# Optimization experiments

Measured on AMD Instinct MI355X. Metric: run time of the kernel, lower is better.

Reference implementation:

```python
import jax, jax.numpy as jnp
import numpy as np

B, T, N, F = 16, 12, 1000, 64
K_CHEB, OUT = 3, 64


def setup_inputs() -> dict:
    key = jax.random.key(0)
    k1, k2, k3, k4 = jax.random.split(key, 4)
    x = jax.random.normal(k1, (B, T, N, F), dtype=jnp.float32)
    SAtt = jax.random.uniform(k2, (B, N, N), dtype=jnp.float32)
    cheb = jax.random.normal(k3, (K_CHEB, N, N), dtype=jnp.float32) * 0.05
    Theta = jax.random.normal(k4, (K_CHEB, F, OUT), dtype=jnp.float32) * 0.05
    return {"x": x, "SAtt": SAtt, "cheb": cheb, "Theta": Theta}


def reference(x, SAtt, cheb, Theta):
    # Attention-masked Chebyshev polynomials: A[b,k,i,j] = cheb[k,i,j] * SAtt[b,i,j]
    A = cheb[None, :, :, :] * SAtt[:, None, :, :]          # (B,K,N,N)
    # rhs[b,t,k,i,f] = sum_j A[b,k,j,i] * x[b,t,j,f]  (transpose of A in original code)
    rhs = jnp.einsum('bkji,btjf->btkif', A, x)             # (B,T,K,N,F)
    # accumulate over k with per-k feature transform Theta[k]
    out = jnp.einsum('btkif,kfo->btio', rhs, Theta)        # (B,T,N,OUT)
    return jax.nn.relu(out)
```

## Files before the change

kernel.cpp:

```cpp
#include <hip/hip_runtime.h>

#define B_  16
#define T_  12
#define N_  1000
#define F_  64
#define KC  3
#define O_  64
#define NP  1024
#define KP  (KC * NP)
#define CC  (T_ * O_)

typedef __bf16 bf16x8 __attribute__((ext_vector_type(8)));
typedef float  f32x4  __attribute__((ext_vector_type(4)));

__device__ __forceinline__ unsigned short f2bf(float f) {
  __bf16 h = (__bf16)f;
  return __builtin_bit_cast(unsigned short, h);
}

__device__ __forceinline__ void gl_lds16(const void* g, void* l) {
  __builtin_amdgcn_global_load_lds(
      (const __attribute__((address_space(1))) unsigned int*)g,
      (__attribute__((address_space(3))) unsigned int*)l,
      16, 0, 0);
}

__global__ __launch_bounds__(256) void k_build_as(
    const float* __restrict__ SAtt, const float* __restrict__ cheb,
    unsigned short* __restrict__ ASt) {
  __shared__ unsigned short prod[KC][64][66];
  const int tid = threadIdx.x;
  const int b = blockIdx.z, ib = blockIdx.x * 64, jb = blockIdx.y * 64;

  const int ii4 = (tid & 15) * 4, jr = tid >> 4;
#pragma unroll
  for (int p = 0; p < 4; ++p) {
    const int jj = p * 16 + jr;
    const int gj = jb + jj;
    const int gjc = gj < N_ ? gj : N_ - 1;
    const int gi = ib + ii4;
    const bool iok = gi < N_;
    const bool ok = iok && (gj < N_);
    float4 s4 = make_float4(0.f, 0.f, 0.f, 0.f);
    if (iok) s4 = *(const float4*)&SAtt[((size_t)b * N_ + gjc) * N_ + gi];
#pragma unroll
    for (int k = 0; k < KC; ++k) {
      float4 c4 = make_float4(0.f, 0.f, 0.f, 0.f);
      if (iok) c4 = *(const float4*)&cheb[((size_t)k * N_ + gjc) * N_ + gi];
      ushort2 lo, hi;
      lo.x = ok ? f2bf(c4.x * s4.x) : (unsigned short)0;
      lo.y = ok ? f2bf(c4.y * s4.y) : (unsigned short)0;
      hi.x = ok ? f2bf(c4.z * s4.z) : (unsigned short)0;
      hi.y = ok ? f2bf(c4.w * s4.w) : (unsigned short)0;
      *(ushort2*)&prod[k][jj][ii4]     = lo;
      *(ushort2*)&prod[k][jj][ii4 + 2] = hi;
    }
  }
  __syncthreads();

  const int j8 = (tid & 7) * 8, i0 = tid >> 3;
#pragma unroll
  for (int p = 0; p < 2; ++p) {
    const int iw = p * 32 + i0;
#pragma unroll
    for (int k = 0; k < KC; ++k) {
      unsigned short v[8];
#pragma unroll
      for (int m = 0; m < 8; ++m) v[m] = prod[k][j8 + m][iw];
      *(uint4*)&ASt[((size_t)(b * NP + ib + iw) * KC + k) * NP + jb + j8] =
          *(uint4*)v;
    }
  }
}

__global__ __launch_bounds__(256) void k_build_y(
    const float* __restrict__ x, const float* __restrict__ Theta,
    unsigned short* __restrict__ Yt) {
  __shared__ unsigned short thl[KC][64][72];
  __shared__ unsigned short xl[128][72];
  __shared__ unsigned short ot[64][136];
  const int tid = threadIdx.x;
  const int bt = blockIdx.y;
  const int jb = blockIdx.x * 128;

#pragma unroll
  for (int it = 0; it < 12; ++it) {
    const int e = (tid + it * 256) * 4;
    const int k = e >> 12, f = (e >> 6) & 63, o0 = e & 63;
    const float4 v = *(const float4*)&Theta[e];
    thl[k][o0 + 0][f] = f2bf(v.x);
    thl[k][o0 + 1][f] = f2bf(v.y);
    thl[k][o0 + 2][f] = f2bf(v.z);
    thl[k][o0 + 3][f] = f2bf(v.w);
  }
  const float* xrow = x + ((size_t)bt * N_ + jb) * F_;
#pragma unroll
  for (int p = 0; p < 8; ++p) {
    const int i4 = tid + p * 256;
    const int fl = i4 * 4, j = fl >> 6, f = fl & 63;
    float4 v;
    if (jb + j < N_) v = ((const float4*)xrow)[i4];
    else             v = make_float4(0.f, 0.f, 0.f, 0.f);
    ushort4 u;
    u.x = f2bf(v.x); u.y = f2bf(v.y); u.z = f2bf(v.z); u.w = f2bf(v.w);
    *(ushort4*)&xl[j][f] = u;
  }
  __syncthreads();

  const int w = tid >> 6, l = tid & 63, quad = l >> 4, lr = l & 15;
  const int o16 = tid >> 4, j8v = (tid & 15) * 8;
#pragma unroll
  for (int k = 0; k < KC; ++k) {
    f32x4 acc[4][2];
#pragma unroll
    for (int mi = 0; mi < 4; ++mi)
#pragma unroll
      for (int ni = 0; ni < 2; ++ni)
        acc[mi][ni] = (f32x4){0.f, 0.f, 0.f, 0.f};
#pragma unroll
    for (int ks = 0; ks < 2; ++ks) {
      const int fo = ks * 32 + quad * 8;
      bf16x8 a[4], bb[2];
#pragma unroll
      for (int mi = 0; mi < 4; ++mi)
        a[mi] = *(const bf16x8*)&thl[k][mi * 16 + lr][fo];
#pragma unroll
      for (int ni = 0; ni < 2; ++ni)
        bb[ni] = *(const bf16x8*)&xl[w * 32 + ni * 16 + lr][fo];
#pragma unroll
      for (int mi = 0; mi < 4; ++mi)
#pragma unroll
        for (int ni = 0; ni < 2; ++ni)
          acc[mi][ni] = __builtin_amdgcn_mfma_f32_16x16x32_bf16(
              a[mi], bb[ni], acc[mi][ni], 0, 0, 0);
    }
    __syncthreads();
#pragma unroll
    for (int mi = 0; mi < 4; ++mi)
#pragma unroll
      for (int ni = 0; ni < 2; ++ni)
#pragma unroll
        for (int r = 0; r < 4; ++r)
          ot[mi * 16 + quad * 4 + r][w * 32 + ni * 16 + lr] =
              f2bf(acc[mi][ni][r]);
    __syncthreads();
#pragma unroll
    for (int oo = 0; oo < 4; ++oo) {
      const int o = oo * 16 + o16;
      const uint4 v = *(const uint4*)&ot[o][j8v];
      *(uint4*)&Yt[((size_t)(bt * O_ + o) * KC + k) * NP + jb + j8v] = v;
    }
  }
}

__global__ __launch_bounds__(256, 2) void k_gemm(
    const unsigned short* __restrict__ ASt, const unsigned short* __restrict__ Yt,
    float* __restrict__ out) {
  __shared__ unsigned short Al[128 * 64];
  __shared__ unsigned short Bl[128 * 64];
  const int tid = threadIdx.x;
  const int bid = blockIdx.x;
  const int xcd = bid & 7, s = bid >> 3;
  const int b = xcd * 2 + (s / 48);
  const int r48 = s % 48;
  const int ib = (r48 / 6) * 128, cb = (r48 % 6) * 128;

  const unsigned short* Abase = ASt + ((size_t)b * NP + ib) * KP;
  const unsigned short* Bbase = Yt + ((size_t)b * CC + cb) * KP;
  const int w = tid >> 6, l = tid & 63, quad = l >> 4, lr = l & 15;
  const int wr = w & 1, wc = w >> 1;
  const int lrow = l >> 3, lchunk = l & 7;
  const int src_chunk = lchunk ^ lrow;
  const int p0 = quad ^ (lr & 7);

  f32x4 acc[4][4];
#pragma unroll
  for (int mi = 0; mi < 4; ++mi)
#pragma unroll
    for (int ci = 0; ci < 4; ++ci)
      acc[mi][ci] = (f32x4){0.f, 0.f, 0.f, 0.f};

  for (int kt = 0; kt < KP / 64; ++kt) {
    __syncthreads();
    const int k0 = kt * 64;
#pragma unroll
    for (int s4 = 0; s4 < 4; ++s4) {
      const int row = w * 32 + s4 * 8;
      gl_lds16(Abase + (size_t)(row + lrow) * KP + k0 + src_chunk * 8,
               &Al[row * 64]);
      gl_lds16(Bbase + (size_t)(row + lrow) * KP + k0 + src_chunk * 8,
               &Bl[row * 64]);
    }
    __syncthreads();
#pragma unroll
    for (int ks = 0; ks < 2; ++ks) {
      const int pc = (p0 ^ (ks * 4)) * 8;
      bf16x8 a[4], bb[4];
#pragma unroll
      for (int mi = 0; mi < 4; ++mi)
        a[mi] = *(const bf16x8*)&Al[(wr * 64 + mi * 16 + lr) * 64 + pc];
#pragma unroll
      for (int ci = 0; ci < 4; ++ci)
        bb[ci] = *(const bf16x8*)&Bl[(wc * 64 + ci * 16 + lr) * 64 + pc];
#pragma unroll
      for (int mi = 0; mi < 4; ++mi)
#pragma unroll
        for (int ci = 0; ci < 4; ++ci)
          acc[mi][ci] = __builtin_amdgcn_mfma_f32_16x16x32_bf16(
              a[mi], bb[ci], acc[mi][ci], 0, 0, 0);
    }
  }

#pragma unroll
  for (int mi = 0; mi < 4; ++mi) {
    const int i = ib + wr * 64 + mi * 16 + quad * 4;
#pragma unroll
    for (int ci = 0; ci < 4; ++ci) {
      const int c = cb + wc * 64 + ci * 16 + lr;
      const int t = c >> 6, o = c & 63;
#pragma unroll
      for (int r = 0; r < 4; ++r) {
        if (i + r < N_) {
          const float v = acc[mi][ci][r];
          out[((size_t)(b * T_ + t) * N_ + (i + r)) * O_ + o] = v > 0.f ? v : 0.f;
        }
      }
    }
  }
}

extern "C" void kernel_launch(void* const* d_in, const int* in_sizes, int n_in,
                              void* d_out, int out_size, void* d_ws, size_t ws_size,
                              hipStream_t stream) {
  const float* x     = (const float*)d_in[0];
  const float* SAtt  = (const float*)d_in[1];
  const float* cheb  = (const float*)d_in[2];
  const float* Theta = (const float*)d_in[3];
  float* out = (float*)d_out;

  unsigned short* ASt = (unsigned short*)d_ws;
  unsigned short* Yt  = ASt + (size_t)B_ * NP * KC * NP;

  k_build_as<<<dim3(16, 16, B_), 256, 0, stream>>>(SAtt, cheb, ASt);
  k_build_y<<<dim3(8, B_ * T_), 256, 0, stream>>>(x, Theta, Yt);
  k_gemm<<<768, 256, 0, stream>>>(ASt, Yt, out);
}
```

Baseline: 321.8 us.

## Load GEMM B operand directly to registers and halve build_y tile

The main GEMM drops the LDS staging buffer for the Yt operand. Each wave now loads its B fragments straight from global memory into registers, which halves shared-memory use and raises the occupancy hint from 2 to 3 blocks per CU. Separately, the Y-building kernel uses 64-row tiles with twice as many blocks to spread that pre-pass wider. The trade-off is that B fragments are no longer shared across the two row-waves, so global or L2 traffic for B goes up, and the direct loads are not swizzled.

```diff
diff --git a/kernel.cpp b/kernel.cpp
--- a/kernel.cpp
+++ b/kernel.cpp
@@ -77,11 +77,11 @@
     const float* __restrict__ x, const float* __restrict__ Theta,
     unsigned short* __restrict__ Yt) {
   __shared__ unsigned short thl[KC][64][72];
-  __shared__ unsigned short xl[128][72];
-  __shared__ unsigned short ot[64][136];
+  __shared__ unsigned short xl[64][72];
+  __shared__ unsigned short ot[64][72];
   const int tid = threadIdx.x;
   const int bt = blockIdx.y;
-  const int jb = blockIdx.x * 128;
+  const int jb = blockIdx.x * 64;
 
 #pragma unroll
   for (int it = 0; it < 12; ++it) {
@@ -95,7 +95,7 @@
   }
   const float* xrow = x + ((size_t)bt * N_ + jb) * F_;
 #pragma unroll
-  for (int p = 0; p < 8; ++p) {
+  for (int p = 0; p < 4; ++p) {
     const int i4 = tid + p * 256;
     const int fl = i4 * 4, j = fl >> 6, f = fl & 63;
     float4 v;
@@ -108,56 +108,39 @@
   __syncthreads();
 
   const int w = tid >> 6, l = tid & 63, quad = l >> 4, lr = l & 15;
-  const int o16 = tid >> 4, j8v = (tid & 15) * 8;
+  const int os = tid >> 2, q = tid & 3;
 #pragma unroll
   for (int k = 0; k < KC; ++k) {
-    f32x4 acc[4][2];
-#pragma unroll
-    for (int mi = 0; mi < 4; ++mi)
-#pragma unroll
-      for (int ni = 0; ni < 2; ++ni)
-        acc[mi][ni] = (f32x4){0.f, 0.f, 0.f, 0.f};
+    f32x4 acc[4];
+#pragma unroll
+    for (int mi = 0; mi < 4; ++mi) acc[mi] = (f32x4){0.f, 0.f, 0.f, 0.f};
 #pragma unroll
     for (int ks = 0; ks < 2; ++ks) {
       const int fo = ks * 32 + quad * 8;
-      bf16x8 a[4], bb[2];
-#pragma unroll
-      for (int mi = 0; mi < 4; ++mi)
-        a[mi] = *(const bf16x8*)&thl[k][mi * 16 + lr][fo];
-#pragma unroll
-      for (int ni = 0; ni < 2; ++ni)
-        bb[ni] = *(const bf16x8*)&xl[w * 32 + ni * 16 + lr][fo];
-#pragma unroll
-      for (int mi = 0; mi < 4; ++mi)
-#pragma unroll
-        for (int ni = 0; ni < 2; ++ni)
-          acc[mi][ni] = __builtin_amdgcn_mfma_f32_16x16x32_bf16(
-              a[mi], bb[ni], acc[mi][ni], 0, 0, 0);
+      const bf16x8 bb = *(const bf16x8*)&xl[w * 16 + lr][fo];
+#pragma unroll
+      for (int mi = 0; mi < 4; ++mi) {
+        const bf16x8 a = *(const bf16x8*)&thl[k][mi * 16 + lr][fo];
+        acc[mi] = __builtin_amdgcn_mfma_f32_16x16x32_bf16(a, bb, acc[mi], 0, 0, 0);
+      }
     }
     __syncthreads();
 #pragma unroll
     for (int mi = 0; mi < 4; ++mi)
 #pragma unroll
-      for (int ni = 0; ni < 2; ++ni)
-#pragma unroll
-        for (int r = 0; r < 4; ++r)
-          ot[mi * 16 + quad * 4 + r][w * 32 + ni * 16 + lr] =
-              f2bf(acc[mi][ni][r]);
-    __syncthreads();
-#pragma unroll
-    for (int oo = 0; oo < 4; ++oo) {
-      const int o = oo * 16 + o16;
-      const uint4 v = *(const uint4*)&ot[o][j8v];
-      *(uint4*)&Yt[((size_t)(bt * O_ + o) * KC + k) * NP + jb + j8v] = v;
-    }
-  }
-}
-
-__global__ __launch_bounds__(256, 2) void k_gemm(
+      for (int r = 0; r < 4; ++r)
+        ot[mi * 16 + quad * 4 + r][w * 16 + lr] = f2bf(acc[mi][r]);
+    __syncthreads();
+    unsigned short* yrow = &Yt[((size_t)(bt * O_ + os) * KC + k) * NP + jb];
+    *(uint4*)&yrow[q * 8]      = *(const uint4*)&ot[os][q * 8];
+    *(uint4*)&yrow[32 + q * 8] = *(const uint4*)&ot[os][32 + q * 8];
+  }
+}
+
+__global__ __launch_bounds__(256, 3) void k_gemm(
     const unsigned short* __restrict__ ASt, const unsigned short* __restrict__ Yt,
     float* __restrict__ out) {
   __shared__ unsigned short Al[128 * 64];
-  __shared__ unsigned short Bl[128 * 64];
   const int tid = threadIdx.x;
   const int bid = blockIdx.x;
   const int xcd = bid & 7, s = bid >> 3;
@@ -166,13 +149,15 @@
   const int ib = (r48 / 6) * 128, cb = (r48 % 6) * 128;
 
   const unsigned short* Abase = ASt + ((size_t)b * NP + ib) * KP;
-  const unsigned short* Bbase = Yt + ((size_t)b * CC + cb) * KP;
   const int w = tid >> 6, l = tid & 63, quad = l >> 4, lr = l & 15;
   const int wr = w & 1, wc = w >> 1;
   const int lrow = l >> 3, lchunk = l & 7;
   const int src_chunk = lchunk ^ lrow;
   const int p0 = quad ^ (lr & 7);
 
+  const unsigned short* Br0 =
+      Yt + ((size_t)(b * CC + cb + wc * 64 + lr)) * KP + quad * 8;
+
   f32x4 acc[4][4];
 #pragma unroll
   for (int mi = 0; mi < 4; ++mi)
@@ -188,26 +173,28 @@
       const int row = w * 32 + s4 * 8;
       gl_lds16(Abase + (size_t)(row + lrow) * KP + k0 + src_chunk * 8,
                &Al[row * 64]);
-      gl_lds16(Bbase + (size_t)(row + lrow) * KP + k0 + src_chunk * 8,
-               &Bl[row * 64]);
-    }
+    }
+    bf16x8 bf[2][4];
+#pragma unroll
+    for (int ks = 0; ks < 2; ++ks)
+#pragma unroll
+      for (int ci = 0; ci < 4; ++ci)
+        bf[ks][ci] =
+            *(const bf16x8*)&Br0[(size_t)ci * 16 * KP + k0 + ks * 32];
     __syncthreads();
 #pragma unroll
     for (int ks = 0; ks < 2; ++ks) {
       const int pc = (p0 ^ (ks * 4)) * 8;
-      bf16x8 a[4], bb[4];
+      bf16x8 a[4];
 #pragma unroll
       for (int mi = 0; mi < 4; ++mi)
         a[mi] = *(const bf16x8*)&Al[(wr * 64 + mi * 16 + lr) * 64 + pc];
 #pragma unroll
-      for (int ci = 0; ci < 4; ++ci)
-        bb[ci] = *(const bf16x8*)&Bl[(wc * 64 + ci * 16 + lr) * 64 + pc];
-#pragma unroll
       for (int mi = 0; mi < 4; ++mi)
 #pragma unroll
         for (int ci = 0; ci < 4; ++ci)
           acc[mi][ci] = __builtin_amdgcn_mfma_f32_16x16x32_bf16(
-              a[mi], bb[ci], acc[mi][ci], 0, 0, 0);
+              a[mi], bf[ks][ci], acc[mi][ci], 0, 0, 0);
     }
   }
 
@@ -242,6 +229,6 @@
   unsigned short* Yt  = ASt + (size_t)B_ * NP * KC * NP;
 
   k_build_as<<<dim3(16, 16, B_), 256, 0, stream>>>(SAtt, cheb, ASt);
-  k_build_y<<<dim3(8, B_ * T_), 256, 0, stream>>>(x, Theta, Yt);
+  k_build_y<<<dim3(16, B_ * T_), 256, 0, stream>>>(x, Theta, Yt);
   k_gemm<<<768, 256, 0, stream>>>(ASt, Yt, out);
 }
```

Result: slower. 389.4 us (+21.0%).
